# Optimization experiments

Measured on AMD Instinct MI355X. Metric: run time of the kernel, lower is better.

The kernel has to match this reference:

```python
import jax, jax.numpy as jnp
import numpy as np

B, T, H, U = 32, 2048, 1024, 1024

def setup_inputs() -> dict:
    key = jax.random.key(0)
    ks = jax.random.split(key, 8)
    s = 1.0 / np.sqrt(H)
    return {
        "dec_hidden": jax.random.normal(ks[0], (B, H), jnp.float32),
        "all_enc_hiddens": jax.random.normal(ks[1], (B, T, H), jnp.float32),
        "W1": jax.random.normal(ks[2], (H, U), jnp.float32) * s,
        "b1": jnp.zeros((U,), jnp.float32),
        "W2": jax.random.normal(ks[3], (H, U), jnp.float32) * s,
        "b2": jnp.zeros((U,), jnp.float32),
        "V": jax.random.normal(ks[4], (U, 1), jnp.float32) * (1.0 / np.sqrt(U)),
        "bv": jnp.zeros((1,), jnp.float32),
    }

def reference(dec_hidden, all_enc_hiddens, W1, b1, W2, b2, V, bv):
    # query projection: [B, 1, U]
    q = (dec_hidden @ W1 + b1)[:, None, :]
    # key projection: [B, T, U]
    k = jnp.einsum("bth,hu->btu", all_enc_hiddens, W2) + b2
    # additive score: [B, T, 1]
    score = jnp.tanh(q + k) @ V + bv
    # softmax over time axis
    attn = jax.nn.softmax(score, axis=1)  # [B, T, 1]
    # weighted context: [B, H]
    context = jnp.sum(attn * all_enc_hiddens, axis=1)
    return (context, attn)
```

## Files before the change

### kernel.cpp

```cpp
#include <hip/hip_runtime.h>
#include <hip/hip_bf16.h>
#include <math.h>

#define B_SZ 32
#define T_SZ 2048
#define H_SZ 1024
#define U_SZ 1024

#define BM 128
#define BN 128
#define BK 64

typedef __attribute__((ext_vector_type(8))) short bf16x8;
typedef __attribute__((ext_vector_type(4))) float f32x4;

__device__ __forceinline__ unsigned int f2bf(float f) {
  union { float f; unsigned int u; } x; x.f = f;
  unsigned int r = x.u + 0x7FFFu + ((x.u >> 16) & 1u);
  return r >> 16;
}

__device__ __forceinline__ void async_cp16(const unsigned short* g, unsigned short* l) {
  __builtin_amdgcn_global_load_lds(
      (const __attribute__((address_space(1))) unsigned int*)g,
      (__attribute__((address_space(3))) unsigned int*)l, 16, 0, 0);
}

__device__ __forceinline__ float fast_tanh(float x) {
  const float e = __expf(x + x);
  return (e - 1.0f) * __builtin_amdgcn_rcpf(e + 1.0f);
}

__global__ void k_cvt_enc(const float* __restrict__ enc, unsigned short* __restrict__ encb) {
  const size_t i = ((size_t)blockIdx.x * 256 + threadIdx.x) * 8;
  const float4 a = *(const float4*)(enc + i);
  const float4 b = *(const float4*)(enc + i + 4);
  uint4 o;
  o.x = f2bf(a.x) | (f2bf(a.y) << 16);
  o.y = f2bf(a.z) | (f2bf(a.w) << 16);
  o.z = f2bf(b.x) | (f2bf(b.y) << 16);
  o.w = f2bf(b.z) | (f2bf(b.w) << 16);
  *(uint4*)(encb + i) = o;
}

__global__ void k_prep_w2t(const float* __restrict__ W2, unsigned short* __restrict__ W2t) {
  __shared__ unsigned short tile[64][65];
  const int bu = blockIdx.x, bh = blockIdx.y;
  const int tc = threadIdx.x & 63, tr = threadIdx.x >> 6;
  #pragma unroll
  for (int i = 0; i < 16; ++i) {
    const int hl = tr + i * 4;
    tile[tc][hl] = (unsigned short)f2bf(W2[(size_t)(bh * 64 + hl) * U_SZ + bu * 64 + tc]);
  }
  __syncthreads();
  #pragma unroll
  for (int i = 0; i < 16; ++i) {
    const int ul = tr + i * 4;
    W2t[(size_t)(bu * 64 + ul) * H_SZ + bh * 64 + tc] = tile[ul][tc];
  }
}

__global__ __launch_bounds__(256) void k_qq(
    const float* __restrict__ dec, const float* __restrict__ W1,
    const float* __restrict__ b1, const float* __restrict__ b2,
    float* __restrict__ qq) {
  __shared__ float red[4][64];
  const int ul = threadIdx.x & 63;
  const int hq = threadIdx.x >> 6;
  const int u  = blockIdx.x * 64 + ul;
  const int b  = blockIdx.y;
  const float* dh = dec + b * H_SZ + hq * 256;
  const float* w  = W1 + (size_t)(hq * 256) * U_SZ + u;
  float acc = 0.0f;
  #pragma unroll 8
  for (int h = 0; h < 256; ++h) acc += dh[h] * w[(size_t)h * U_SZ];
  red[hq][ul] = acc;
  __syncthreads();
  if (threadIdx.x < 64) {
    const float s = red[0][ul] + red[1][ul] + red[2][ul] + red[3][ul];
    qq[b * U_SZ + u] = s + b1[u] + b2[u];
  }
}

template <bool PRE_BF16>
__global__ __launch_bounds__(256) void k_gemm_score(
    const unsigned short* __restrict__ encb,
    const float* __restrict__ encf,
    const unsigned short* __restrict__ W2t,
    const float* __restrict__ qq, const float* __restrict__ Vv,
    float* __restrict__ score)
{
  __shared__ unsigned short Al[BM * BK];
  __shared__ unsigned short Bl[BN * BK];
  __shared__ float scoreS[BM];

  const int tid  = threadIdx.x;
  const int wave = tid >> 6;
  const int lane = tid & 63;
  const int quad = lane >> 4;
  const int l16  = lane & 15;
  const int wr   = wave >> 1;
  const int wc   = wave & 1;
  const int m0   = blockIdx.x * BM;
  const int b    = m0 >> 11;

  if (tid < BM) scoreS[tid] = 0.0f;

  size_t aoff[4], boff[4];
  unsigned short *dstA[4], *dstB[4];
  #pragma unroll
  for (int i = 0; i < 4; ++i) {
    const int slot = (i * 4 + wave) * 64 + lane;
    const int r = slot >> 3;
    const int c = ((slot & 7) - r) & 7;
    aoff[i] = (size_t)(m0 + r) * H_SZ + c * 8;
    boff[i] = (size_t)r * H_SZ + c * 8;
    dstA[i] = &Al[(i * 4 + wave) * 512];
    dstB[i] = &Bl[(i * 4 + wave) * 512];
  }

  const int ar[4] = { wr * 64 + 0 * 16 + l16, wr * 64 + 1 * 16 + l16,
                      wr * 64 + 2 * 16 + l16, wr * 64 + 3 * 16 + l16 };
  const int bu[4] = { wc * 64 + 0 * 16 + l16, wc * 64 + 1 * 16 + l16,
                      wc * 64 + 2 * 16 + l16, wc * 64 + 3 * 16 + l16 };

  for (int ut = 0; ut < 8; ++ut) {
    const int u0 = ut * BN;
    f32x4 acc[4][4];
    #pragma unroll
    for (int rt = 0; rt < 4; ++rt)
      #pragma unroll
      for (int ct = 0; ct < 4; ++ct)
        #pragma unroll
        for (int r = 0; r < 4; ++r) acc[rt][ct][r] = 0.0f;

    for (int kk = 0; kk < H_SZ; kk += BK) {
      __syncthreads();
      if constexpr (PRE_BF16) {
        #pragma unroll
        for (int i = 0; i < 4; ++i) async_cp16(encb + aoff[i] + kk, dstA[i]);
      } else {
        #pragma unroll
        for (int i = 0; i < 4; ++i) {
          const int slot = i * 256 + tid;
          const int r = slot >> 3;
          const int c = ((slot & 7) - r) & 7;
          const float* src = encf + (size_t)(m0 + r) * H_SZ + kk + c * 8;
          const float4 x = *(const float4*)src;
          const float4 y = *(const float4*)(src + 4);
          uint4 o;
          o.x = f2bf(x.x) | (f2bf(x.y) << 16);
          o.y = f2bf(x.z) | (f2bf(x.w) << 16);
          o.z = f2bf(y.x) | (f2bf(y.y) << 16);
          o.w = f2bf(y.z) | (f2bf(y.w) << 16);
          *(uint4*)&Al[slot * 8] = o;
        }
      }
      #pragma unroll
      for (int i = 0; i < 4; ++i)
        async_cp16(W2t + (size_t)u0 * H_SZ + boff[i] + kk, dstB[i]);
      __syncthreads();

      #pragma unroll
      for (int h = 0; h < 2; ++h) {
        bf16x8 af[4], bfr[4];
        #pragma unroll
        for (int rt = 0; rt < 4; ++rt)
          af[rt] = *(const bf16x8*)&Al[ar[rt] * 64 + ((h * 4 + quad + ar[rt]) & 7) * 8];
        #pragma unroll
        for (int ct = 0; ct < 4; ++ct)
          bfr[ct] = *(const bf16x8*)&Bl[bu[ct] * 64 + ((h * 4 + quad + bu[ct]) & 7) * 8];
        #pragma unroll
        for (int rt = 0; rt < 4; ++rt)
          #pragma unroll
          for (int ct = 0; ct < 4; ++ct)
            acc[rt][ct] = __builtin_amdgcn_mfma_f32_16x16x32_bf16(
                af[rt], bfr[ct], acc[rt][ct], 0, 0, 0);
      }
    }

    float part[4][4];
    #pragma unroll
    for (int rt = 0; rt < 4; ++rt)
      #pragma unroll
      for (int r = 0; r < 4; ++r) part[rt][r] = 0.0f;
    #pragma unroll
    for (int ct = 0; ct < 4; ++ct) {
      const int u = u0 + wc * 64 + ct * 16 + l16;
      const float qv = qq[b * U_SZ + u];
      const float vv = Vv[u];
      #pragma unroll
      for (int rt = 0; rt < 4; ++rt)
        #pragma unroll
        for (int r = 0; r < 4; ++r)
          part[rt][r] += fast_tanh(acc[rt][ct][r] + qv) * vv;
    }
    #pragma unroll
    for (int rt = 0; rt < 4; ++rt)
      #pragma unroll
      for (int r = 0; r < 4; ++r) {
        float p = part[rt][r];
        p += __shfl_xor(p, 1);
        p += __shfl_xor(p, 2);
        p += __shfl_xor(p, 4);
        p += __shfl_xor(p, 8);
        part[rt][r] = p;
      }
    if (l16 == 0) {
      #pragma unroll
      for (int rt = 0; rt < 4; ++rt)
        #pragma unroll
        for (int r = 0; r < 4; ++r)
          atomicAdd(&scoreS[wr * 64 + rt * 16 + quad * 4 + r], part[rt][r]);
    }
  }
  __syncthreads();
  if (tid < BM) score[m0 + tid] = scoreS[tid];
}

__global__ void k_softmax(const float* __restrict__ score, float* __restrict__ attn) {
  const int b = blockIdx.x;
  const int tid = threadIdx.x;
  __shared__ float wmax[4], wsum[4];
  const float* s = score + b * T_SZ;
  float v[8];
  float lmax = -INFINITY;
  #pragma unroll
  for (int i = 0; i < 8; ++i) { v[i] = s[tid + i * 256]; lmax = fmaxf(lmax, v[i]); }
  #pragma unroll
  for (int m = 1; m <= 32; m <<= 1) lmax = fmaxf(lmax, __shfl_xor(lmax, m));
  if ((tid & 63) == 0) wmax[tid >> 6] = lmax;
  __syncthreads();
  const float gmax = fmaxf(fmaxf(wmax[0], wmax[1]), fmaxf(wmax[2], wmax[3]));
  float lsum = 0.0f;
  #pragma unroll
  for (int i = 0; i < 8; ++i) { v[i] = __expf(v[i] - gmax); lsum += v[i]; }
  #pragma unroll
  for (int m = 1; m <= 32; m <<= 1) lsum += __shfl_xor(lsum, m);
  if ((tid & 63) == 0) wsum[tid >> 6] = lsum;
  __syncthreads();
  const float inv = 1.0f / (wsum[0] + wsum[1] + wsum[2] + wsum[3]);
  #pragma unroll
  for (int i = 0; i < 8; ++i) attn[b * T_SZ + tid + i * 256] = v[i] * inv;
}

__global__ void k_context(const float* __restrict__ enc, const float* __restrict__ attn,
                          float* __restrict__ ctx) {
  const int tcx = blockIdx.x;
  const int hc  = blockIdx.y;
  const int b   = blockIdx.z;
  const int h   = hc * 256 + threadIdx.x;
  const float* e = enc + ((size_t)b * T_SZ + tcx * 256) * H_SZ + h;
  const float* a = attn + b * T_SZ + tcx * 256;
  float a0 = 0, a1 = 0, a2 = 0, a3 = 0;
  for (int t = 0; t < 256; t += 4) {
    a0 += a[t]     * e[(size_t)t * H_SZ];
    a1 += a[t + 1] * e[(size_t)(t + 1) * H_SZ];
    a2 += a[t + 2] * e[(size_t)(t + 2) * H_SZ];
    a3 += a[t + 3] * e[(size_t)(t + 3) * H_SZ];
  }
  atomicAdd(&ctx[b * H_SZ + h], (a0 + a1) + (a2 + a3));
}

extern "C" void kernel_launch(void* const* d_in, const int* in_sizes, int n_in,
                              void* d_out, int out_size, void* d_ws, size_t ws_size,
                              hipStream_t stream) {
  const float* dec = (const float*)d_in[0];
  const float* enc = (const float*)d_in[1];
  const float* W1  = (const float*)d_in[2];
  const float* b1  = (const float*)d_in[3];
  const float* W2  = (const float*)d_in[4];
  const float* b2  = (const float*)d_in[5];
  const float* Vv  = (const float*)d_in[6];

  const size_t encb_bytes = (size_t)B_SZ * T_SZ * H_SZ * 2;
  const size_t fast_need  = encb_bytes + (2u << 20) + (128u << 10) + (256u << 10);
  const bool fast = ws_size >= fast_need;

  char* ws = (char*)d_ws;
  unsigned short* encb = nullptr;
  unsigned short* W2t;
  float *qq, *score;
  if (fast) {
    encb  = (unsigned short*)ws;
    W2t   = (unsigned short*)(ws + encb_bytes);
    qq    = (float*)(ws + encb_bytes + (2u << 20));
    score = (float*)(ws + encb_bytes + (2u << 20) + (128u << 10));
  } else {
    W2t   = (unsigned short*)ws;
    qq    = (float*)(ws + (2u << 20));
    score = (float*)(ws + (2u << 20) + (128u << 10));
  }

  float* ctx  = (float*)d_out;
  float* attn = (float*)d_out + B_SZ * H_SZ;

  hipMemsetAsync(ctx, 0, B_SZ * H_SZ * sizeof(float), stream);
  if (fast)
    k_cvt_enc<<<(B_SZ * T_SZ * H_SZ) / (256 * 8), 256, 0, stream>>>(enc, encb);
  k_prep_w2t<<<dim3(16, 16), 256, 0, stream>>>(W2, W2t);
  k_qq<<<dim3(16, 32), 256, 0, stream>>>(dec, W1, b1, b2, qq);
  if (fast)
    k_gemm_score<true><<<(B_SZ * T_SZ) / BM, 256, 0, stream>>>(encb, enc, W2t, qq, Vv, score);
  else
    k_gemm_score<false><<<(B_SZ * T_SZ) / BM, 256, 0, stream>>>(encb, enc, W2t, qq, Vv, score);
  k_softmax<<<32, 256, 0, stream>>>(score, attn);
  k_context<<<dim3(8, 4, 32), 256, 0, stream>>>(enc, attn, ctx);
}
```

Measured before the change: 654.5 us.

## Retile score GEMM, merge prep kernels, read bf16 encoder copy for context

Changes the score GEMM tile from 128x128 to 64x256, so each wave owns a 64-column slice across all 64 rows, with 4 U-tiles instead of 8. Merges the encoder conversion, W2 transpose and query projection into one launch to cut launch overhead. The context reduction now reads the bf16 encoder copy instead of fp32, halving its memory traffic, at some precision cost in the context output. The new tiling changes how A and B are reused and how blocks are spread over the grid, with twice as many blocks.

```diff
diff --git a/kernel.cpp b/kernel.cpp
--- a/kernel.cpp
+++ b/kernel.cpp
@@ -7,9 +7,10 @@
 #define H_SZ 1024
 #define U_SZ 1024
 
-#define BM 128
-#define BN 128
+#define BM 64
+#define BN 256
 #define BK 64
+#define UT_N (U_SZ / BN)
 
 typedef __attribute__((ext_vector_type(8))) short bf16x8;
 typedef __attribute__((ext_vector_type(4))) float f32x4;
@@ -20,6 +21,10 @@
   return r >> 16;
 }
 
+__device__ __forceinline__ float bf2f(unsigned int lo16) {
+  union { unsigned int u; float f; } x; x.u = lo16 << 16; return x.f;
+}
+
 __device__ __forceinline__ void async_cp16(const unsigned short* g, unsigned short* l) {
   __builtin_amdgcn_global_load_lds(
       (const __attribute__((address_space(1))) unsigned int*)g,
@@ -31,54 +36,61 @@
   return (e - 1.0f) * __builtin_amdgcn_rcpf(e + 1.0f);
 }
 
-__global__ void k_cvt_enc(const float* __restrict__ enc, unsigned short* __restrict__ encb) {
-  const size_t i = ((size_t)blockIdx.x * 256 + threadIdx.x) * 8;
-  const float4 a = *(const float4*)(enc + i);
-  const float4 b = *(const float4*)(enc + i + 4);
-  uint4 o;
-  o.x = f2bf(a.x) | (f2bf(a.y) << 16);
-  o.y = f2bf(a.z) | (f2bf(a.w) << 16);
-  o.z = f2bf(b.x) | (f2bf(b.y) << 16);
-  o.w = f2bf(b.z) | (f2bf(b.w) << 16);
-  *(uint4*)(encb + i) = o;
-}
-
-__global__ void k_prep_w2t(const float* __restrict__ W2, unsigned short* __restrict__ W2t) {
-  __shared__ unsigned short tile[64][65];
-  const int bu = blockIdx.x, bh = blockIdx.y;
-  const int tc = threadIdx.x & 63, tr = threadIdx.x >> 6;
-  #pragma unroll
-  for (int i = 0; i < 16; ++i) {
-    const int hl = tr + i * 4;
-    tile[tc][hl] = (unsigned short)f2bf(W2[(size_t)(bh * 64 + hl) * U_SZ + bu * 64 + tc]);
-  }
-  __syncthreads();
-  #pragma unroll
-  for (int i = 0; i < 16; ++i) {
-    const int ul = tr + i * 4;
-    W2t[(size_t)(bu * 64 + ul) * H_SZ + bh * 64 + tc] = tile[ul][tc];
-  }
-}
-
-__global__ __launch_bounds__(256) void k_qq(
+__global__ __launch_bounds__(256) void k_prep(
+    const float* __restrict__ enc, unsigned short* __restrict__ encb,
+    const float* __restrict__ W2, unsigned short* __restrict__ W2t,
     const float* __restrict__ dec, const float* __restrict__ W1,
     const float* __restrict__ b1, const float* __restrict__ b2,
-    float* __restrict__ qq) {
-  __shared__ float red[4][64];
-  const int ul = threadIdx.x & 63;
-  const int hq = threadIdx.x >> 6;
-  const int u  = blockIdx.x * 64 + ul;
-  const int b  = blockIdx.y;
-  const float* dh = dec + b * H_SZ + hq * 256;
-  const float* w  = W1 + (size_t)(hq * 256) * U_SZ + u;
-  float acc = 0.0f;
-  #pragma unroll 8
-  for (int h = 0; h < 256; ++h) acc += dh[h] * w[(size_t)h * U_SZ];
-  red[hq][ul] = acc;
-  __syncthreads();
-  if (threadIdx.x < 64) {
-    const float s = red[0][ul] + red[1][ul] + red[2][ul] + red[3][ul];
-    qq[b * U_SZ + u] = s + b1[u] + b2[u];
+    float* __restrict__ qq, int cvtN)
+{
+  __shared__ char lds_raw[64 * 65 * 2];
+  const int bid = blockIdx.x;
+  const int tid = threadIdx.x;
+
+  if (bid < cvtN) {
+    const size_t i = ((size_t)bid * 256 + tid) * 8;
+    const float4 a = *(const float4*)(enc + i);
+    const float4 b = *(const float4*)(enc + i + 4);
+    uint4 o;
+    o.x = f2bf(a.x) | (f2bf(a.y) << 16);
+    o.y = f2bf(a.z) | (f2bf(a.w) << 16);
+    o.z = f2bf(b.x) | (f2bf(b.y) << 16);
+    o.w = f2bf(b.z) | (f2bf(b.w) << 16);
+    *(uint4*)(encb + i) = o;
+  } else if (bid < cvtN + 256) {
+    unsigned short (*tile)[65] = (unsigned short(*)[65])lds_raw;
+    const int idx = bid - cvtN;
+    const int bu = idx & 15, bh = idx >> 4;
+    const int tc = tid & 63, tr = tid >> 6;
+    #pragma unroll
+    for (int i = 0; i < 16; ++i) {
+      const int hl = tr + i * 4;
+      tile[tc][hl] = (unsigned short)f2bf(W2[(size_t)(bh * 64 + hl) * U_SZ + bu * 64 + tc]);
+    }
+    __syncthreads();
+    #pragma unroll
+    for (int i = 0; i < 16; ++i) {
+      const int ul = tr + i * 4;
+      W2t[(size_t)(bu * 64 + ul) * H_SZ + bh * 64 + tc] = tile[ul][tc];
+    }
+  } else {
+    float (*red)[64] = (float(*)[64])lds_raw;
+    const int idx = bid - (cvtN + 256);
+    const int ul = tid & 63;
+    const int hq = tid >> 6;
+    const int u  = (idx & 15) * 64 + ul;
+    const int b  = idx >> 4;
+    const float* dh = dec + b * H_SZ + hq * 256;
+    const float* w  = W1 + (size_t)(hq * 256) * U_SZ + u;
+    float acc = 0.0f;
+    #pragma unroll 8
+    for (int h = 0; h < 256; ++h) acc += dh[h] * w[(size_t)h * U_SZ];
+    red[hq][ul] = acc;
+    __syncthreads();
+    if (tid < 64) {
+      const float s = red[0][ul] + red[1][ul] + red[2][ul] + red[3][ul];
+      qq[b * U_SZ + u] = s + b1[u] + b2[u];
+    }
   }
 }
 
@@ -99,32 +111,35 @@
   const int lane = tid & 63;
   const int quad = lane >> 4;
   const int l16  = lane & 15;
-  const int wr   = wave >> 1;
-  const int wc   = wave & 1;
   const int m0   = blockIdx.x * BM;
   const int b    = m0 >> 11;
 
   if (tid < BM) scoreS[tid] = 0.0f;
 
-  size_t aoff[4], boff[4];
-  unsigned short *dstA[4], *dstB[4];
-  #pragma unroll
-  for (int i = 0; i < 4; ++i) {
+  size_t aoff[2]; unsigned short* dstA[2];
+  #pragma unroll
+  for (int i = 0; i < 2; ++i) {
     const int slot = (i * 4 + wave) * 64 + lane;
     const int r = slot >> 3;
     const int c = ((slot & 7) - r) & 7;
     aoff[i] = (size_t)(m0 + r) * H_SZ + c * 8;
+    dstA[i] = &Al[(i * 4 + wave) * 512];
+  }
+  size_t boff[8]; unsigned short* dstB[8];
+  #pragma unroll
+  for (int i = 0; i < 8; ++i) {
+    const int slot = (i * 4 + wave) * 64 + lane;
+    const int r = slot >> 3;
+    const int c = ((slot & 7) - r) & 7;
     boff[i] = (size_t)r * H_SZ + c * 8;
-    dstA[i] = &Al[(i * 4 + wave) * 512];
     dstB[i] = &Bl[(i * 4 + wave) * 512];
   }
 
-  const int ar[4] = { wr * 64 + 0 * 16 + l16, wr * 64 + 1 * 16 + l16,
-                      wr * 64 + 2 * 16 + l16, wr * 64 + 3 * 16 + l16 };
-  const int bu[4] = { wc * 64 + 0 * 16 + l16, wc * 64 + 1 * 16 + l16,
-                      wc * 64 + 2 * 16 + l16, wc * 64 + 3 * 16 + l16 };
-
-  for (int ut = 0; ut < 8; ++ut) {
+  const int ar[4] = { 0 * 16 + l16, 1 * 16 + l16, 2 * 16 + l16, 3 * 16 + l16 };
+  const int bu[4] = { wave * 64 + 0 * 16 + l16, wave * 64 + 1 * 16 + l16,
+                      wave * 64 + 2 * 16 + l16, wave * 64 + 3 * 16 + l16 };
+
+  for (int ut = 0; ut < UT_N; ++ut) {
     const int u0 = ut * BN;
     f32x4 acc[4][4];
     #pragma unroll
@@ -138,10 +153,10 @@
       __syncthreads();
       if constexpr (PRE_BF16) {
         #pragma unroll
-        for (int i = 0; i < 4; ++i) async_cp16(encb + aoff[i] + kk, dstA[i]);
+        for (int i = 0; i < 2; ++i) async_cp16(encb + aoff[i] + kk, dstA[i]);
       } else {
         #pragma unroll
-        for (int i = 0; i < 4; ++i) {
+        for (int i = 0; i < 2; ++i) {
           const int slot = i * 256 + tid;
           const int r = slot >> 3;
           const int c = ((slot & 7) - r) & 7;
@@ -157,7 +172,7 @@
         }
       }
       #pragma unroll
-      for (int i = 0; i < 4; ++i)
+      for (int i = 0; i < 8; ++i)
         async_cp16(W2t + (size_t)u0 * H_SZ + boff[i] + kk, dstB[i]);
       __syncthreads();
 
@@ -186,7 +201,7 @@
       for (int r = 0; r < 4; ++r) part[rt][r] = 0.0f;
     #pragma unroll
     for (int ct = 0; ct < 4; ++ct) {
-      const int u = u0 + wc * 64 + ct * 16 + l16;
+      const int u = u0 + wave * 64 + ct * 16 + l16;
       const float qv = qq[b * U_SZ + u];
       const float vv = Vv[u];
       #pragma unroll
@@ -211,7 +226,7 @@
       for (int rt = 0; rt < 4; ++rt)
         #pragma unroll
         for (int r = 0; r < 4; ++r)
-          atomicAdd(&scoreS[wr * 64 + rt * 16 + quad * 4 + r], part[rt][r]);
+          atomicAdd(&scoreS[rt * 16 + quad * 4 + r], part[rt][r]);
     }
   }
   __syncthreads();
@@ -244,12 +259,29 @@
   for (int i = 0; i < 8; ++i) attn[b * T_SZ + tid + i * 256] = v[i] * inv;
 }
 
-__global__ void k_context(const float* __restrict__ enc, const float* __restrict__ attn,
-                          float* __restrict__ ctx) {
+__global__ void k_context_bf16(const unsigned short* __restrict__ encb,
+                               const float* __restrict__ attn, float* __restrict__ ctx) {
   const int tcx = blockIdx.x;
   const int hc  = blockIdx.y;
   const int b   = blockIdx.z;
-  const int h   = hc * 256 + threadIdx.x;
+  const int h0  = hc * 512 + threadIdx.x * 2;
+  const unsigned short* e = encb + ((size_t)b * T_SZ + tcx * 256) * H_SZ + h0;
+  const float* a = attn + b * T_SZ + tcx * 256;
+  float c0 = 0, c1 = 0;
+  #pragma unroll 4
+  for (int t = 0; t < 256; ++t) {
+    const unsigned int v = *(const unsigned int*)&e[(size_t)t * H_SZ];
+    c0 += a[t] * bf2f(v & 0xFFFFu);
+    c1 += a[t] * bf2f(v >> 16);
+  }
+  atomicAdd(&ctx[b * H_SZ + h0],     c0);
+  atomicAdd(&ctx[b * H_SZ + h0 + 1], c1);
+}
+
+__global__ void k_context_f32(const float* __restrict__ enc,
+                              const float* __restrict__ attn, float* __restrict__ ctx) {
+  const int tcx = blockIdx.x, hc = blockIdx.y, b = blockIdx.z;
+  const int h = hc * 256 + threadIdx.x;
   const float* e = enc + ((size_t)b * T_SZ + tcx * 256) * H_SZ + h;
   const float* a = attn + b * T_SZ + tcx * 256;
   float a0 = 0, a1 = 0, a2 = 0, a3 = 0;
@@ -296,14 +328,16 @@
   float* attn = (float*)d_out + B_SZ * H_SZ;
 
   hipMemsetAsync(ctx, 0, B_SZ * H_SZ * sizeof(float), stream);
-  if (fast)
-    k_cvt_enc<<<(B_SZ * T_SZ * H_SZ) / (256 * 8), 256, 0, stream>>>(enc, encb);
-  k_prep_w2t<<<dim3(16, 16), 256, 0, stream>>>(W2, W2t);
-  k_qq<<<dim3(16, 32), 256, 0, stream>>>(dec, W1, b1, b2, qq);
+  const int cvtN = fast ? (B_SZ * T_SZ * H_SZ) / (256 * 8) : 0;
+  k_prep<<<cvtN + 256 + 512, 256, 0, stream>>>(enc, encb, W2, W2t,
+                                               dec, W1, b1, b2, qq, cvtN);
   if (fast)
     k_gemm_score<true><<<(B_SZ * T_SZ) / BM, 256, 0, stream>>>(encb, enc, W2t, qq, Vv, score);
   else
     k_gemm_score<false><<<(B_SZ * T_SZ) / BM, 256, 0, stream>>>(encb, enc, W2t, qq, Vv, score);
   k_softmax<<<32, 256, 0, stream>>>(score, attn);
-  k_context<<<dim3(8, 4, 32), 256, 0, stream>>>(enc, attn, ctx);
-}
+  if (fast)
+    k_context_bf16<<<dim3(8, 2, 32), 256, 0, stream>>>(encb, attn, ctx);
+  else
+    k_context_f32<<<dim3(8, 4, 32), 256, 0, stream>>>(enc, attn, ctx);
+}
```

After: 636.9 us. -2.7%, faster.
